# Kernel tuning notes

Hardware: AMD Instinct MI355X
Metric: run time of the kernel (lower is better)

The kernel has to match this reference:

```python
import jax, jax.numpy as jnp
import numpy as np

BS, SLEN, DIM, N_HEADS = 2, 2048, 2048, 16
DH = DIM // N_HEADS


def setup_inputs() -> dict:
    key = jax.random.key(0)
    ks = jax.random.split(key, 10)
    s = DIM ** -0.5
    x = jax.random.normal(ks[0], (BS, SLEN, DIM), dtype=jnp.float32)
    # causal attention mask from get_masks: True = attend
    mask = jnp.tril(jnp.ones((SLEN, SLEN), dtype=bool))[None].repeat(BS, axis=0)
    Wq = jax.random.normal(ks[1], (DIM, DIM), jnp.float32) * s
    bq = jnp.zeros((DIM,), jnp.float32)
    Wk = jax.random.normal(ks[2], (DIM, DIM), jnp.float32) * s
    bk = jnp.zeros((DIM,), jnp.float32)
    Wv = jax.random.normal(ks[3], (DIM, DIM), jnp.float32) * s
    bv = jnp.zeros((DIM,), jnp.float32)
    Wo = jax.random.normal(ks[4], (DIM, DIM), jnp.float32) * s
    bo = jnp.zeros((DIM,), jnp.float32)
    # normalized_attention learned scalar, init 1/sqrt(dim_per_head)
    scale = jnp.asarray(1.0 / np.sqrt(DH), dtype=jnp.float32)
    return {"x": x, "mask": mask, "Wq": Wq, "bq": bq, "Wk": Wk, "bk": bk,
            "Wv": Wv, "bv": bv, "Wo": Wo, "bo": bo, "scale": scale}


def _split_heads(t):  # (bs, slen, dim) -> (bs, H, slen, dh)
    return t.reshape(BS, -1, N_HEADS, DH).transpose(0, 2, 1, 3)


def reference(x, mask, Wq, bq, Wk, bk, Wv, bv, Wo, bo, scale):
    # QKV projections (torch Linear: x @ W.T + b)
    q = _split_heads(x @ Wq.T + bq)
    k = _split_heads(x @ Wk.T + bk)
    v = _split_heads(x @ Wv.T + bv)
    # normalized attention: L2-normalize q, k on head dim, learned scalar scale
    q = q / jnp.linalg.norm(q, axis=-1, keepdims=True)
    k = k / jnp.linalg.norm(k, axis=-1, keepdims=True)
    q = q * scale
    scores = jnp.einsum('bhqd,bhkd->bhqk', q, k)  # (bs, H, qlen, klen)
    scores = jnp.where(mask[:, None, :, :], scores, -jnp.inf)
    weights = jax.nn.softmax(scores, axis=-1)  # dropout p=0 / eval
    ctx = jnp.einsum('bhqk,bhkd->bhqd', weights, v)
    ctx = ctx.transpose(0, 2, 1, 3).reshape(BS, SLEN, DIM)
    return ctx @ Wo.T + bo
```

## Files before the change

kernel.cpp:

```cpp
#include <hip/hip_runtime.h>
#include <hip/hip_bf16.h>

#define S_LEN 2048
#define DIMN  2048
#define NHEAD 16
#define DHEAD 128
#define SEGQ  ((size_t)4096 * 2048)
#define SEGW  ((size_t)2048 * 2048)

typedef __attribute__((ext_vector_type(8))) short short8;
typedef __attribute__((ext_vector_type(4))) float floatx4;

__device__ inline float bf2f(unsigned short u) {
    union { unsigned int i; float f; } v; v.i = ((unsigned int)u) << 16; return v.f;
}
__device__ inline unsigned short f2bf(float f) {
    unsigned int x = __float_as_uint(f);
    unsigned int r = (x + 0x7FFFu + ((x >> 16) & 1u)) >> 16;
    return (unsigned short)r;
}
__device__ inline short8 ld8_f32_as_bf16(const float* p) {
    float4 a = *(const float4*)p;
    float4 b = *(const float4*)(p + 4);
    short8 r;
    r[0] = (short)f2bf(a.x); r[1] = (short)f2bf(a.y);
    r[2] = (short)f2bf(a.z); r[3] = (short)f2bf(a.w);
    r[4] = (short)f2bf(b.x); r[5] = (short)f2bf(b.y);
    r[6] = (short)f2bf(b.z); r[7] = (short)f2bf(b.w);
    return r;
}
__device__ inline void glds16(unsigned short* lds, const unsigned short* g) {
    __builtin_amdgcn_global_load_lds(
        (const __attribute__((address_space(1))) unsigned int*)g,
        (__attribute__((address_space(3))) unsigned int*)lds, 16, 0, 0);
}

__global__ __launch_bounds__(256) void cvt5_kernel(
    const float* __restrict__ s0, const float* __restrict__ s1,
    const float* __restrict__ s2, const float* __restrict__ s3,
    const float* __restrict__ s4,
    unsigned short* __restrict__ d0, unsigned short* __restrict__ d1,
    unsigned short* __restrict__ d2, unsigned short* __restrict__ d3,
    unsigned short* __restrict__ d4)
{
    const float* s; unsigned short* d; size_t n;
    switch (blockIdx.y) {
        case 0:  s = s0; d = d0; n = SEGQ; break;
        case 1:  s = s1; d = d1; n = SEGW; break;
        case 2:  s = s2; d = d2; n = SEGW; break;
        case 3:  s = s3; d = d3; n = SEGW; break;
        default: s = s4; d = d4; n = SEGW; break;
    }
    size_t stride = (size_t)gridDim.x * 256 * 8;
    for (size_t i = ((size_t)blockIdx.x * 256 + threadIdx.x) * 8; i < n; i += stride)
        *(short8*)&d[i] = ld8_f32_as_bf16(&s[i]);
}

template <int EPI>
__global__ __launch_bounds__(256) void gemm_glds(
    const unsigned short* __restrict__ A, const unsigned short* __restrict__ Bw,
    const float* __restrict__ b0, const float* __restrict__ b1,
    const float* __restrict__ b2, const float* __restrict__ scale_p,
    void* __restrict__ Cp, int M, int N, int K)
{
    __shared__ __align__(16) unsigned short sA[128 * 32];
    __shared__ __align__(16) unsigned short sB[128 * 32];

    const int tid  = threadIdx.x;
    const int w    = tid >> 6, lane = tid & 63;
    const int l15  = lane & 15, quad = lane >> 4;
    const int wm   = w >> 1, wn = w & 1;
    const int tm   = blockIdx.y * 128, tn = blockIdx.x * 128;
    const int lrow = lane >> 2;
    const int kcol = (lane & 3) * 8;

    floatx4 acc[4][4] = {};

    for (int k0 = 0; k0 < K; k0 += 32) {
        __syncthreads();
#pragma unroll
        for (int i = 0; i < 2; i++) {
            int r0 = w * 32 + i * 16;
            glds16(&sA[r0 * 32], &A[(size_t)(tm + r0 + lrow) * K + k0 + kcol]);
            glds16(&sB[r0 * 32], &Bw[(size_t)(tn + r0 + lrow) * K + k0 + kcol]);
        }
        __syncthreads();

        short8 af[4], bfr[4];
#pragma unroll
        for (int mi = 0; mi < 4; mi++)
            af[mi] = *(const short8*)&sA[(wm * 64 + mi * 16 + l15) * 32 + quad * 8];
#pragma unroll
        for (int ni = 0; ni < 4; ni++)
            bfr[ni] = *(const short8*)&sB[(wn * 64 + ni * 16 + l15) * 32 + quad * 8];
#pragma unroll
        for (int mi = 0; mi < 4; mi++)
#pragma unroll
            for (int ni = 0; ni < 4; ni++)
                acc[mi][ni] = __builtin_amdgcn_mfma_f32_16x16x32_bf16(af[mi], bfr[ni], acc[mi][ni], 0, 0, 0);
    }

    if (EPI == 0) {
        const int t = tn >> 11;
        const float* bp = (t == 0) ? b0 : (t == 1) ? b1 : b2;
        unsigned short* Q = (unsigned short*)Cp;
#pragma unroll
        for (int ni = 0; ni < 4; ni++) {
            int n = tn + wn * 64 + ni * 16 + l15;
            float bias = bp[n & 2047];
#pragma unroll
            for (int mi = 0; mi < 4; mi++)
#pragma unroll
                for (int r = 0; r < 4; r++) acc[mi][ni][r] += bias;
        }
        float ssq[4][4];
#pragma unroll
        for (int mi = 0; mi < 4; mi++)
#pragma unroll
            for (int r = 0; r < 4; r++) {
                float s = 0.0f;
#pragma unroll
                for (int ni = 0; ni < 4; ni++) s += acc[mi][ni][r] * acc[mi][ni][r];
#pragma unroll
                for (int off = 1; off < 16; off <<= 1) s += __shfl_xor(s, off, 64);
                ssq[mi][r] = s;
            }
        __syncthreads();
        float* ssh = (float*)sA;
        if (l15 == 0) {
#pragma unroll
            for (int mi = 0; mi < 4; mi++)
#pragma unroll
                for (int r = 0; r < 4; r++)
                    ssh[wn * 128 + wm * 64 + mi * 16 + quad * 4 + r] = ssq[mi][r];
        }
        __syncthreads();
        const float scl = (t == 0) ? scale_p[0] : 1.0f;
#pragma unroll
        for (int mi = 0; mi < 4; mi++) {
            int mbase = tm + wm * 64 + mi * 16 + quad * 4;
#pragma unroll
            for (int r = 0; r < 4; r++) {
                float tot = ssq[mi][r] + ssh[(wn ^ 1) * 128 + wm * 64 + mi * 16 + quad * 4 + r];
                float f = (t < 2) ? rsqrtf(tot) * scl : 1.0f;
                int m = mbase + r;
                int b = m >> 11, s = m & 2047;
#pragma unroll
                for (int ni = 0; ni < 4; ni++) {
                    int n = tn + wn * 64 + ni * 16 + l15;
                    int h = (n >> 7) & 15, dh = n & 127;
                    float v = acc[mi][ni][r] * f;
                    size_t idx = (t < 2)
                        ? (size_t)t * SEGQ + (((size_t)(b * NHEAD + h)) * S_LEN + s) * DHEAD + dh
                        : 2 * SEGQ + (((size_t)(b * NHEAD + h)) * DHEAD + dh) * S_LEN + s;
                    Q[idx] = f2bf(v);
                }
            }
        }
    } else {
#pragma unroll
        for (int mi = 0; mi < 4; mi++) {
            int mbase = tm + wm * 64 + mi * 16 + quad * 4;
#pragma unroll
            for (int ni = 0; ni < 4; ni++) {
                int n = tn + wn * 64 + ni * 16 + l15;
                float bias = b0[n];
#pragma unroll
                for (int r = 0; r < 4; r++) {
                    int m = mbase + r;
                    ((float*)Cp)[(size_t)m * N + n] = acc[mi][ni][r] + bias;
                }
            }
        }
    }
}

template <int SPLIT, int A_F32, int OUT_F32>
__global__ __launch_bounds__(256) void gemm_bt(
    const void* __restrict__ Ap, const float* __restrict__ Bw,
    const float* __restrict__ bias, void* __restrict__ Cp,
    int M, int N, int K)
{
    __shared__ __align__(16) unsigned short sA[128 * 40];
    __shared__ __align__(16) unsigned short sB[128 * 40];

    const int tid  = threadIdx.x;
    const int w    = tid >> 6, lane = tid & 63;
    const int l15  = lane & 15, quad = lane >> 4;
    const int wm   = w >> 1, wn = w & 1;
    const int tm   = blockIdx.y * 128, tn = blockIdx.x * 128;

    const float*          Af32 = (const float*)Ap;
    const unsigned short* Abf  = (const unsigned short*)Ap;

    floatx4 acc[4][4] = {};

    for (int k0 = 0; k0 < K; k0 += 32) {
        __syncthreads();
#pragma unroll
        for (int i = 0; i < 2; i++) {
            int c   = tid + i * 256;
            int row = c >> 2;
            int kc  = (c & 3) * 8;
            size_t goff = (size_t)(tm + row) * K + k0 + kc;
            if (A_F32)
                *(short8*)&sA[row * 40 + kc] = ld8_f32_as_bf16(&Af32[goff]);
            else
                *(short8*)&sA[row * 40 + kc] = *(const short8*)&Abf[goff];
            *(short8*)&sB[row * 40 + kc] =
                ld8_f32_as_bf16(&Bw[(size_t)(tn + row) * K + k0 + kc]);
        }
        __syncthreads();

        short8 af[4], bfr[4];
#pragma unroll
        for (int mi = 0; mi < 4; mi++)
            af[mi] = *(const short8*)&sA[(wm * 64 + mi * 16 + l15) * 40 + quad * 8];
#pragma unroll
        for (int ni = 0; ni < 4; ni++)
            bfr[ni] = *(const short8*)&sB[(wn * 64 + ni * 16 + l15) * 40 + quad * 8];
#pragma unroll
        for (int mi = 0; mi < 4; mi++)
#pragma unroll
            for (int ni = 0; ni < 4; ni++)
                acc[mi][ni] = __builtin_amdgcn_mfma_f32_16x16x32_bf16(af[mi], bfr[ni], acc[mi][ni], 0, 0, 0);
    }

#pragma unroll
    for (int mi = 0; mi < 4; mi++) {
        int mbase = tm + wm * 64 + mi * 16 + quad * 4;
#pragma unroll
        for (int ni = 0; ni < 4; ni++) {
            int n = tn + wn * 64 + ni * 16 + l15;
            float bv = bias[n];
#pragma unroll
            for (int r = 0; r < 4; r++) {
                int m = mbase + r;
                float v = acc[mi][ni][r] + bv;
                if (SPLIT == 1) {
                    int b = m >> 11, s = m & 2047, h = n >> 7, dh = n & 127;
                    ((unsigned short*)Cp)[(((size_t)(b * NHEAD + h)) * S_LEN + s) * DHEAD + dh] = f2bf(v);
                } else if (SPLIT == 2) {
                    int b = m >> 11, s = m & 2047, h = n >> 7, dh = n & 127;
                    ((unsigned short*)Cp)[(((size_t)(b * NHEAD + h)) * DHEAD + dh) * S_LEN + s] = f2bf(v);
                } else if (OUT_F32) {
                    ((float*)Cp)[(size_t)m * N + n] = v;
                } else {
                    ((unsigned short*)Cp)[(size_t)m * N + n] = f2bf(v);
                }
            }
        }
    }
}

__global__ __launch_bounds__(256) void l2norm_kernel(
    unsigned short* __restrict__ qn, unsigned short* __restrict__ kn,
    const float* __restrict__ scale_p)
{
    const int w = threadIdx.x >> 6, lane = threadIdx.x & 63;
    size_t row = (size_t)blockIdx.x * 4 + w;
    unsigned short* base = (blockIdx.y == 0 ? qn : kn) + row * DHEAD;
    float a = bf2f(base[lane * 2]);
    float b = bf2f(base[lane * 2 + 1]);
    float ss = a * a + b * b;
#pragma unroll
    for (int off = 1; off < 64; off <<= 1) ss += __shfl_xor(ss, off, 64);
    float f = rsqrtf(ss);
    if (blockIdx.y == 0) f *= scale_p[0];
    base[lane * 2]     = f2bf(a * f);
    base[lane * 2 + 1] = f2bf(b * f);
}

#define KSTR  136
#define VTSTR 136
#define PSTR  136

__global__ __launch_bounds__(512) void attn_kernel4(
    const unsigned short* __restrict__ qn, const unsigned short* __restrict__ kn,
    const unsigned short* __restrict__ vt, unsigned short* __restrict__ ctx)
{
    __shared__ __align__(16) unsigned short sK [128 * KSTR];
    __shared__ __align__(16) unsigned short sVt[128 * VTSTR];
    __shared__ __align__(16) unsigned short sP [8 * 16 * PSTR];

    const int tid  = threadIdx.x;
    const int w    = tid >> 6, lane = tid & 63;
    const int l15  = lane & 15, quad = lane >> 4;
    const int xb   = blockIdx.x, bh = blockIdx.y;
    const size_t headoff = (size_t)bh * S_LEN * DHEAD;
    const unsigned short* kbase0 = kn + headoff;
    const unsigned short* vtbase = vt + headoff;
    unsigned short* sPw = sP + w * 16 * PSTR;

    short8 kpre[4], vpre[4];

    for (int half = 0; half < 2; half++) {
        const int qt = half ? (15 - xb) : xb;

        const unsigned short* qrow = qn + headoff + (size_t)(qt * 128 + w * 16 + l15) * DHEAD;
        short8 aQ[4];
#pragma unroll
        for (int ks = 0; ks < 4; ks++) aQ[ks] = *(const short8*)(qrow + ks * 32 + quad * 8);

        floatx4 O[8] = {};
        float m_i[4], l_i[4];
#pragma unroll
        for (int r = 0; r < 4; r++) { m_i[r] = -1e30f; l_i[r] = 0.0f; }

        if (half == 0) {
#pragma unroll
            for (int j = 0; j < 4; j++) {
                int c = tid + j * 512;
                kpre[j] = *(const short8*)(kbase0 + (size_t)(c >> 4) * DHEAD + (c & 15) * 8);
                vpre[j] = *(const short8*)(vtbase + (size_t)(c >> 4) * S_LEN + (c & 15) * 8);
            }
        }

        for (int kt = 0; kt <= qt; kt++) {
            __syncthreads();

#pragma unroll
            for (int j = 0; j < 4; j++) {
                int c = tid + j * 512;
                *(short8*)&sK [(c >> 4) * KSTR  + (c & 15) * 8] = kpre[j];
                *(short8*)&sVt[(c >> 4) * VTSTR + (c & 15) * 8] = vpre[j];
            }

            if (kt < qt || half == 0) {
                const int knext = (kt < qt) ? (kt + 1) * 128 : 0;
#pragma unroll
                for (int j = 0; j < 4; j++) {
                    int c = tid + j * 512;
                    kpre[j] = *(const short8*)(kbase0 + (size_t)(knext + (c >> 4)) * DHEAD + (c & 15) * 8);
                    vpre[j] = *(const short8*)(vtbase + (size_t)(c >> 4) * S_LEN + knext + (c & 15) * 8);
                }
            }
            __syncthreads();

            floatx4 sc[8] = {};
#pragma unroll
            for (int ks = 0; ks < 4; ks++) {
#pragma unroll
                for (int ni = 0; ni < 8; ni++) {
                    short8 bK = *(const short8*)&sK[(ni * 16 + l15) * KSTR + ks * 32 + quad * 8];
                    sc[ni] = __builtin_amdgcn_mfma_f32_16x16x32_bf16(aQ[ks], bK, sc[ni], 0, 0, 0);
                }
            }

            if (kt == qt) {
#pragma unroll
                for (int ni = 0; ni < 8; ni++) {
                    int cl = ni * 16 + l15;
#pragma unroll
                    for (int r = 0; r < 4; r++) {
                        int rl = w * 16 + quad * 4 + r;
                        if (cl > rl) sc[ni][r] = -1e30f;
                    }
                }
            }

            float rmax[4];
#pragma unroll
            for (int r = 0; r < 4; r++) {
                float mx = sc[0][r];
#pragma unroll
                for (int ni = 1; ni < 8; ni++) mx = fmaxf(mx, sc[ni][r]);
                rmax[r] = mx;
            }
#pragma unroll
            for (int off = 1; off < 16; off <<= 1)
#pragma unroll
                for (int r = 0; r < 4; r++) rmax[r] = fmaxf(rmax[r], __shfl_xor(rmax[r], off, 64));

            float alpha[4], rsum[4];
#pragma unroll
            for (int r = 0; r < 4; r++) {
                float mn = fmaxf(m_i[r], rmax[r]);
                alpha[r] = exp2f((m_i[r] - mn) * 1.44269504f);
                m_i[r] = mn;
                rsum[r] = 0.0f;
            }
#pragma unroll
            for (int ni = 0; ni < 8; ni++) {
#pragma unroll
                for (int r = 0; r < 4; r++) {
                    float p = exp2f((sc[ni][r] - m_i[r]) * 1.44269504f);
                    rsum[r] += p;
                    sPw[(quad * 4 + r) * PSTR + ni * 16 + l15] = f2bf(p);
                }
            }
#pragma unroll
            for (int off = 1; off < 16; off <<= 1)
#pragma unroll
                for (int r = 0; r < 4; r++) rsum[r] += __shfl_xor(rsum[r], off, 64);
#pragma unroll
            for (int r = 0; r < 4; r++) l_i[r] = l_i[r] * alpha[r] + rsum[r];
#pragma unroll
            for (int t = 0; t < 8; t++)
#pragma unroll
                for (int r = 0; r < 4; r++) O[t][r] *= alpha[r];

            __syncthreads();

#pragma unroll
            for (int ks2 = 0; ks2 < 4; ks2++) {
                short8 aP = *(const short8*)&sPw[l15 * PSTR + ks2 * 32 + quad * 8];
#pragma unroll
                for (int t = 0; t < 8; t++) {
                    short8 bV = *(const short8*)&sVt[(t * 16 + l15) * VTSTR + ks2 * 32 + quad * 8];
                    O[t] = __builtin_amdgcn_mfma_f32_16x16x32_bf16(aP, bV, O[t], 0, 0, 0);
                }
            }
        }

        const int b = bh >> 4, h = bh & 15;
#pragma unroll
        for (int r = 0; r < 4; r++) {
            float inv = 1.0f / l_i[r];
            int srow = qt * 128 + w * 16 + quad * 4 + r;
            size_t rowoff = ((size_t)(b * S_LEN + srow)) * DIMN + h * DHEAD;
#pragma unroll
            for (int t = 0; t < 8; t++)
                ctx[rowoff + t * 16 + l15] = f2bf(O[t][r] * inv);
        }
    }
}

extern "C" void kernel_launch(void* const* d_in, const int* in_sizes, int n_in,
                              void* d_out, int out_size, void* d_ws, size_t ws_size,
                              hipStream_t stream)
{
    const float* x     = (const float*)d_in[0];
    const float* Wq    = (const float*)d_in[2];
    const float* bq    = (const float*)d_in[3];
    const float* Wk    = (const float*)d_in[4];
    const float* bk    = (const float*)d_in[5];
    const float* Wv    = (const float*)d_in[6];
    const float* bv    = (const float*)d_in[7];
    const float* Wo    = (const float*)d_in[8];
    const float* bo    = (const float*)d_in[9];
    const float* scale = (const float*)d_in[10];

    const int M = 4096, N = 2048, K = 2048;
    float* out = (float*)d_out;
    const size_t need = (SEGQ + 4 * SEGW + 3 * SEGQ) * sizeof(unsigned short);

    if (ws_size >= need) {
        unsigned short* xb  = (unsigned short*)d_ws;
        unsigned short* wqb = xb  + SEGQ;
        unsigned short* wkb = wqb + SEGW;
        unsigned short* wvb = wkb + SEGW;
        unsigned short* wob = wvb + SEGW;
        unsigned short* qn  = wob + SEGW;
        unsigned short* kn  = qn  + SEGQ;
        unsigned short* vtb = kn  + SEGQ;
        unsigned short* ctx = xb;

        cvt5_kernel<<<dim3(512, 5), 256, 0, stream>>>(x, Wq, Wk, Wv, Wo,
                                                      xb, wqb, wkb, wvb, wob);
        gemm_glds<0><<<dim3(48, 32), 256, 0, stream>>>(xb, wqb, bq, bk, bv, scale, qn, M, 6144, K);
        attn_kernel4<<<dim3(8, 32), 512, 0, stream>>>(qn, kn, vtb, ctx);
        gemm_glds<1><<<dim3(16, 32), 256, 0, stream>>>(ctx, wob, bo, nullptr, nullptr, nullptr, out, M, N, K);
    } else {
        unsigned short* qn  = (unsigned short*)d_ws;
        unsigned short* kn  = qn + SEGQ;
        unsigned short* vtb = kn + SEGQ;
        unsigned short* ctx = vtb + SEGQ;

        gemm_bt<1, 1, 0><<<dim3(16, 32), 256, 0, stream>>>(x, Wq, bq, qn, M, N, K);
        gemm_bt<1, 1, 0><<<dim3(16, 32), 256, 0, stream>>>(x, Wk, bk, kn, M, N, K);
        gemm_bt<2, 1, 0><<<dim3(16, 32), 256, 0, stream>>>(x, Wv, bv, vtb, M, N, K);
        l2norm_kernel<<<dim3(16384, 2), 256, 0, stream>>>(qn, kn, scale);
        attn_kernel4<<<dim3(8, 32), 512, 0, stream>>>(qn, kn, vtb, ctx);
        gemm_bt<0, 0, 1><<<dim3(16, 32), 256, 0, stream>>>(ctx, Wo, bo, out, M, N, K);
    }
}
```

Measured before the change: 472.3 us.

## Triple-buffer GEMM LDS loads with 256x128 tiles and swizzled layout

Replaces the synchronous single-buffer bf16 GEMM with a 512-thread, 256x128-tile kernel that keeps three LDS stages in flight. Direct global-to-LDS loads are issued two k-steps ahead and tracked with explicit vmcnt waits, so memory latency overlaps MFMA work. The LDS column index is XOR-swizzled to reduce bank conflicts, and MFMA sections run at raised wave priority. The cost is a larger LDS footprint, which limits occupancy, and fewer blocks in the grid, which may hurt load balance across CUs.

```diff
diff --git a/kernel.cpp b/kernel.cpp
--- a/kernel.cpp
+++ b/kernel.cpp
@@ -56,49 +56,73 @@
         *(short8*)&d[i] = ld8_f32_as_bf16(&s[i]);
 }
 
+#define BUFE (384 * 32)
+
 template <int EPI>
-__global__ __launch_bounds__(256) void gemm_glds(
+__global__ __launch_bounds__(512) void gemm3(
     const unsigned short* __restrict__ A, const unsigned short* __restrict__ Bw,
     const float* __restrict__ b0, const float* __restrict__ b1,
     const float* __restrict__ b2, const float* __restrict__ scale_p,
     void* __restrict__ Cp, int M, int N, int K)
 {
-    __shared__ __align__(16) unsigned short sA[128 * 32];
-    __shared__ __align__(16) unsigned short sB[128 * 32];
+    __shared__ __align__(16) unsigned short sBuf[3 * BUFE];
 
     const int tid  = threadIdx.x;
     const int w    = tid >> 6, lane = tid & 63;
     const int l15  = lane & 15, quad = lane >> 4;
-    const int wm   = w >> 1, wn = w & 1;
-    const int tm   = blockIdx.y * 128, tn = blockIdx.x * 128;
-    const int lrow = lane >> 2;
-    const int kcol = (lane & 3) * 8;
+    const int wr   = w >> 1, wc = w & 1;
+    const int tm   = blockIdx.y * 256, tn = blockIdx.x * 128;
+
+    const int colE = ((lane & 3) * 8) ^ (((lane >> 3) & 3) << 3);
+    const int cs   = (quad * 8) ^ (((l15 >> 1) & 3) << 3);
+    const int srow = w * 16 + (lane >> 2);
 
     floatx4 acc[4][4] = {};
 
-    for (int k0 = 0; k0 < K; k0 += 32) {
-        __syncthreads();
-#pragma unroll
-        for (int i = 0; i < 2; i++) {
-            int r0 = w * 32 + i * 16;
-            glds16(&sA[r0 * 32], &A[(size_t)(tm + r0 + lrow) * K + k0 + kcol]);
-            glds16(&sB[r0 * 32], &Bw[(size_t)(tn + r0 + lrow) * K + k0 + kcol]);
-        }
-        __syncthreads();
-
+    auto stage = [&](int kt, int bsel) {
+        const int k0 = kt * 32;
+        glds16(&sBuf[bsel * BUFE + 0 * 4096 + w * 512],
+               &A[(size_t)(tm + srow) * K + k0 + colE]);
+        glds16(&sBuf[bsel * BUFE + 1 * 4096 + w * 512],
+               &A[(size_t)(tm + 128 + srow) * K + k0 + colE]);
+        glds16(&sBuf[bsel * BUFE + 8192 + w * 512],
+               &Bw[(size_t)(tn + srow) * K + k0 + colE]);
+    };
+
+    const int nT = K >> 5;
+    stage(0, 0);
+    stage(1, 1);
+
+    int bs = 0;
+    for (int t = 0; t < nT; ++t) {
+        if (t < nT - 1) asm volatile("s_waitcnt vmcnt(3)" ::: "memory");
+        else            asm volatile("s_waitcnt vmcnt(0)" ::: "memory");
+        __builtin_amdgcn_s_barrier();
+        __builtin_amdgcn_sched_barrier(0);
+
+        const unsigned short* bufA = &sBuf[bs * BUFE];
+        const unsigned short* bufB = bufA + 8192;
         short8 af[4], bfr[4];
 #pragma unroll
         for (int mi = 0; mi < 4; mi++)
-            af[mi] = *(const short8*)&sA[(wm * 64 + mi * 16 + l15) * 32 + quad * 8];
+            af[mi] = *(const short8*)&bufA[(wr * 64 + mi * 16 + l15) * 32 + cs];
 #pragma unroll
         for (int ni = 0; ni < 4; ni++)
-            bfr[ni] = *(const short8*)&sB[(wn * 64 + ni * 16 + l15) * 32 + quad * 8];
+            bfr[ni] = *(const short8*)&bufB[(wc * 64 + ni * 16 + l15) * 32 + cs];
+
+        if (t + 2 < nT) stage(t + 2, bs == 0 ? 2 : bs - 1);
+
+        __builtin_amdgcn_s_setprio(1);
 #pragma unroll
         for (int mi = 0; mi < 4; mi++)
 #pragma unroll
             for (int ni = 0; ni < 4; ni++)
                 acc[mi][ni] = __builtin_amdgcn_mfma_f32_16x16x32_bf16(af[mi], bfr[ni], acc[mi][ni], 0, 0, 0);
-    }
+        __builtin_amdgcn_s_setprio(0);
+
+        bs = (bs == 2) ? 0 : bs + 1;
+    }
+    __syncthreads();
 
     if (EPI == 0) {
         const int t = tn >> 11;
@@ -106,7 +130,7 @@
         unsigned short* Q = (unsigned short*)Cp;
 #pragma unroll
         for (int ni = 0; ni < 4; ni++) {
-            int n = tn + wn * 64 + ni * 16 + l15;
+            int n = tn + wc * 64 + ni * 16 + l15;
             float bias = bp[n & 2047];
 #pragma unroll
             for (int mi = 0; mi < 4; mi++)
@@ -125,29 +149,28 @@
                 for (int off = 1; off < 16; off <<= 1) s += __shfl_xor(s, off, 64);
                 ssq[mi][r] = s;
             }
-        __syncthreads();
-        float* ssh = (float*)sA;
+        float* ssh = (float*)sBuf;
         if (l15 == 0) {
 #pragma unroll
             for (int mi = 0; mi < 4; mi++)
 #pragma unroll
                 for (int r = 0; r < 4; r++)
-                    ssh[wn * 128 + wm * 64 + mi * 16 + quad * 4 + r] = ssq[mi][r];
+                    ssh[wc * 256 + wr * 64 + mi * 16 + quad * 4 + r] = ssq[mi][r];
         }
         __syncthreads();
         const float scl = (t == 0) ? scale_p[0] : 1.0f;
 #pragma unroll
         for (int mi = 0; mi < 4; mi++) {
-            int mbase = tm + wm * 64 + mi * 16 + quad * 4;
+            int mbase = tm + wr * 64 + mi * 16 + quad * 4;
 #pragma unroll
             for (int r = 0; r < 4; r++) {
-                float tot = ssq[mi][r] + ssh[(wn ^ 1) * 128 + wm * 64 + mi * 16 + quad * 4 + r];
+                float tot = ssq[mi][r] + ssh[(wc ^ 1) * 256 + wr * 64 + mi * 16 + quad * 4 + r];
                 float f = (t < 2) ? rsqrtf(tot) * scl : 1.0f;
                 int m = mbase + r;
                 int b = m >> 11, s = m & 2047;
 #pragma unroll
                 for (int ni = 0; ni < 4; ni++) {
-                    int n = tn + wn * 64 + ni * 16 + l15;
+                    int n = tn + wc * 64 + ni * 16 + l15;
                     int h = (n >> 7) & 15, dh = n & 127;
                     float v = acc[mi][ni][r] * f;
                     size_t idx = (t < 2)
@@ -160,10 +183,10 @@
     } else {
 #pragma unroll
         for (int mi = 0; mi < 4; mi++) {
-            int mbase = tm + wm * 64 + mi * 16 + quad * 4;
+            int mbase = tm + wr * 64 + mi * 16 + quad * 4;
 #pragma unroll
             for (int ni = 0; ni < 4; ni++) {
-                int n = tn + wn * 64 + ni * 16 + l15;
+                int n = tn + wc * 64 + ni * 16 + l15;
                 float bias = b0[n];
 #pragma unroll
                 for (int r = 0; r < 4; r++) {
@@ -458,9 +481,9 @@
 
         cvt5_kernel<<<dim3(512, 5), 256, 0, stream>>>(x, Wq, Wk, Wv, Wo,
                                                       xb, wqb, wkb, wvb, wob);
-        gemm_glds<0><<<dim3(48, 32), 256, 0, stream>>>(xb, wqb, bq, bk, bv, scale, qn, M, 6144, K);
+        gemm3<0><<<dim3(48, 16), 512, 0, stream>>>(xb, wqb, bq, bk, bv, scale, qn, M, 6144, K);
         attn_kernel4<<<dim3(8, 32), 512, 0, stream>>>(qn, kn, vtb, ctx);
-        gemm_glds<1><<<dim3(16, 32), 256, 0, stream>>>(ctx, wob, bo, nullptr, nullptr, nullptr, out, M, N, K);
+        gemm3<1><<<dim3(16, 16), 512, 0, stream>>>(ctx, wob, bo, nullptr, nullptr, nullptr, out, M, N, K);
     } else {
         unsigned short* qn  = (unsigned short*)d_ws;
         unsigned short* kn  = qn + SEGQ;
```

Result: faster. 430.2 us (-8.9%).
